# Optimization experiments

Hardware: AMD Instinct MI355X
Metric: run time of the kernel (lower is better)

## Reference

```python
import jax, jax.numpy as jnp
import numpy as np

# Modulated deformable conv2d (torchvision semantics): per kernel tap, sample the
# input at a runtime-offset location via bilinear interpolation (zero padding
# outside the image), modulate with mask, then do the weighted accumulation.

STRIDE = (1, 1)
PADDING = (1, 1)
DILATION = (1, 1)


def deform_conv2d(x, offset, mask, weight, bias):
    B, C, H, W = x.shape
    O, Cg, kh, kw = weight.shape
    K = kh * kw
    og = offset.shape[1] // (2 * K)          # offset groups
    Ho, Wo = offset.shape[2], offset.shape[3]
    sh, sw = STRIDE
    ph, pw = PADDING
    dh, dw = DILATION

    off = offset.reshape(B, og, K, 2, Ho, Wo)
    ki = jnp.arange(K)
    base_ky = ((ki // kw) * dh).astype(x.dtype)            # [K]
    base_kx = ((ki % kw) * dw).astype(x.dtype)
    base_h = (jnp.arange(Ho) * sh - ph).astype(x.dtype)    # [Ho]
    base_w = (jnp.arange(Wo) * sw - pw).astype(x.dtype)    # [Wo]
    # sampling positions, [B, og, K, Ho, Wo]
    p_y = off[:, :, :, 0] + base_ky[None, None, :, None, None] + base_h[None, None, None, :, None]
    p_x = off[:, :, :, 1] + base_kx[None, None, :, None, None] + base_w[None, None, None, None, :]

    y0 = jnp.floor(p_y)
    x0 = jnp.floor(p_x)
    ly = p_y - y0
    lx = p_x - x0
    y0i = y0.astype(jnp.int32)
    x0i = x0.astype(jnp.int32)

    Cog = C // og
    x_flat = x.reshape(B, og, Cog, H * W)

    def gather(yi, xi):
        valid = ((yi >= 0) & (yi < H) & (xi >= 0) & (xi < W))
        idx = jnp.clip(yi, 0, H - 1) * W + jnp.clip(xi, 0, W - 1)
        idx_flat = idx.reshape(B, og, 1, K * Ho * Wo)
        v = jnp.take_along_axis(x_flat, idx_flat, axis=3).reshape(B, og, Cog, K, Ho, Wo)
        return v * valid[:, :, None].astype(x.dtype)

    w00 = ((1 - ly) * (1 - lx))[:, :, None]
    w01 = ((1 - ly) * lx)[:, :, None]
    w10 = (ly * (1 - lx))[:, :, None]
    w11 = (ly * lx)[:, :, None]
    val = (w00 * gather(y0i, x0i) + w01 * gather(y0i, x0i + 1)
           + w10 * gather(y0i + 1, x0i) + w11 * gather(y0i + 1, x0i + 1))

    if mask is not None:
        val = val * mask.reshape(B, og, K, Ho, Wo)[:, :, None]

    # grouped conv accumulation over sampled taps
    G = C // Cg                               # conv groups (=1 here)
    val = val.reshape(B, G, C // G, K, Ho, Wo)
    w = weight.reshape(G, O // G, Cg, K)
    out = jnp.einsum('bgckhw,gock->bgohw', val, w).reshape(B, O, Ho, Wo)
    if bias is not None:
        out = out + bias[None, :, None, None]
    return out


def setup_inputs() -> dict:
    key = jax.random.key(0)
    k1, k2, k3, k4, k5 = jax.random.split(key, 5)
    B, C, H, W = 4, 64, 128, 128
    O, kh, kw = 64, 3, 3
    return {
        'input': jax.random.normal(k1, (B, C, H, W), dtype=jnp.float32),
        'offset': jax.random.normal(k2, (B, 2 * kh * kw, H, W), dtype=jnp.float32),
        'mask': jax.random.uniform(k3, (B, kh * kw, H, W), dtype=jnp.float32),
        'weight': jax.random.normal(k4, (O, C, kh, kw), dtype=jnp.float32) * (1.0 / np.sqrt(C * kh * kw)),
        'bias': jax.random.normal(k5, (O,), dtype=jnp.float32) * 0.01,
    }


def reference(input, offset, mask, weight, bias):
    return deform_conv2d(input, offset, mask, weight, bias)
```

## Files before the change

kernel.cpp:

```cpp
#include <hip/hip_runtime.h>


#define BB 4
#define CC 64
#define HH 128
#define WW 128
#define OO 64
#define KHW 3
#define KK 9
#define HW (HH * WW)

typedef __bf16 bf16_t;
typedef bf16_t bf16x8 __attribute__((ext_vector_type(8)));
typedef float f32x4 __attribute__((ext_vector_type(4)));

__global__ __launch_bounds__(256) void nhwc_kernel(const float* __restrict__ x,
                                                   bf16_t* __restrict__ xt) {
    __shared__ float tile[64 * 65];
    const int t  = threadIdx.x;
    const int b  = blockIdx.x >> 8;
    const int p0 = (blockIdx.x & 255) << 6;
#pragma unroll
    for (int i = 0; i < 16; ++i) {
        int c = i * 4 + (t >> 6);
        int p = t & 63;
        tile[c * 65 + p] = x[(b * CC + c) * HW + p0 + p];
    }
    __syncthreads();
#pragma unroll
    for (int i = 0; i < 16; ++i) {
        int p = i * 4 + (t >> 6);
        int c = t & 63;
        xt[(size_t)((b * HW) + p0 + p) * CC + c] = (bf16_t)tile[c * 65 + p];
    }
}

__global__ void wfrag_kernel(const float* __restrict__ w,
                             bf16_t* __restrict__ wf) {
    int i = blockIdx.x * blockDim.x + threadIdx.x;
    if (i >= OO * CC * KK) return;
    int j    = i & 7;
    int lane = (i >> 3) & 63;
    int nt   = (i >> 9) & 3;
    int q    = (i >> 11) & 1;
    int k    = i >> 12;
    int o = nt * 16 + (lane & 15);
    int c = q * 32 + ((lane >> 4) << 3) + j;
    wf[i] = (bf16_t)w[(o * CC + c) * KK + k];
}

__global__ __launch_bounds__(256, 2) void deform_conv_mfma(
    const bf16_t* __restrict__ xt, const float* __restrict__ offset,
    const float* __restrict__ mask, const bf16x8* __restrict__ wf,
    const float* __restrict__ bias, float* __restrict__ out) {
    const int t    = threadIdx.x;
    const int b    = blockIdx.x >> 8;
    const int p0   = (blockIdx.x & 255) << 6;
    const int lane = t & 63;
    const int wv   = t >> 6;
    const int m0   = wv << 4;
    const int col  = lane & 15;
    const int quad = lane >> 4;

    const int rem = p0 + m0 + col;
    const int ho  = rem >> 7;
    const int wo  = rem & (WW - 1);
    const int chq = quad << 3;

    const bf16_t* xb = xt + (size_t)b * HW * CC;

    f32x4 acc[4];
#pragma unroll
    for (int nt = 0; nt < 4; ++nt) acc[nt] = (f32x4){0.f, 0.f, 0.f, 0.f};

    for (int k = 0; k < KK; ++k) {
        float offy = offset[((b * (2 * KK) + 2 * k) * HW) + rem];
        float offx = offset[((b * (2 * KK) + 2 * k + 1) * HW) + rem];
        float mm   = mask[((b * KK + k) * HW) + rem];
        float py = offy + (float)(k / KHW) + (float)(ho - 1);
        float px = offx + (float)(k % KHW) + (float)(wo - 1);
        float fy0 = floorf(py), fx0 = floorf(px);
        float ly = py - fy0, lx = px - fx0;
        int y0 = (int)fy0, x0 = (int)fx0;
        int y1 = y0 + 1, x1 = x0 + 1;
        bool vy0 = (y0 >= 0) && (y0 < HH);
        bool vy1 = (y1 >= 0) && (y1 < HH);
        bool vx0 = (x0 >= 0) && (x0 < WW);
        bool vx1 = (x1 >= 0) && (x1 < WW);
        int cy0 = min(max(y0, 0), HH - 1), cy1 = min(max(y1, 0), HH - 1);
        int cx0 = min(max(x0, 0), WW - 1), cx1 = min(max(x1, 0), WW - 1);
        float w0 = (vy0 && vx0) ? mm * (1.0f - ly) * (1.0f - lx) : 0.0f;
        float w1 = (vy0 && vx1) ? mm * (1.0f - ly) * lx : 0.0f;
        float w2 = (vy1 && vx0) ? mm * ly * (1.0f - lx) : 0.0f;
        float w3 = (vy1 && vx1) ? mm * ly * lx : 0.0f;

        const bf16_t* c00 = xb + (cy0 * WW + cx0) * CC + chq;
        const bf16_t* c01 = xb + (cy0 * WW + cx1) * CC + chq;
        const bf16_t* c10 = xb + (cy1 * WW + cx0) * CC + chq;
        const bf16_t* c11 = xb + (cy1 * WW + cx1) * CC + chq;

        bf16x8 a00 = *(const bf16x8*)(c00);
        bf16x8 a01 = *(const bf16x8*)(c01);
        bf16x8 a02 = *(const bf16x8*)(c10);
        bf16x8 a03 = *(const bf16x8*)(c11);
        bf16x8 a10 = *(const bf16x8*)(c00 + 32);
        bf16x8 a11 = *(const bf16x8*)(c01 + 32);
        bf16x8 a12 = *(const bf16x8*)(c10 + 32);
        bf16x8 a13 = *(const bf16x8*)(c11 + 32);

        bf16x8 af0, af1;
#pragma unroll
        for (int i = 0; i < 8; ++i) {
            float v = w0 * (float)a00[i] + w1 * (float)a01[i] +
                      w2 * (float)a02[i] + w3 * (float)a03[i];
            af0[i] = (bf16_t)v;
        }
#pragma unroll
        for (int i = 0; i < 8; ++i) {
            float v = w0 * (float)a10[i] + w1 * (float)a11[i] +
                      w2 * (float)a12[i] + w3 * (float)a13[i];
            af1[i] = (bf16_t)v;
        }

        const bf16x8* wk = wf + (size_t)(k * 8) * 64;
#pragma unroll
        for (int nt = 0; nt < 4; ++nt) {
            bf16x8 b0 = wk[nt * 64 + lane];
            acc[nt] = __builtin_amdgcn_mfma_f32_16x16x32_bf16(af0, b0, acc[nt],
                                                              0, 0, 0);
        }
#pragma unroll
        for (int nt = 0; nt < 4; ++nt) {
            bf16x8 b1 = wk[(4 + nt) * 64 + lane];
            acc[nt] = __builtin_amdgcn_mfma_f32_16x16x32_bf16(af1, b1, acc[nt],
                                                              0, 0, 0);
        }
    }

#pragma unroll
    for (int nt = 0; nt < 4; ++nt) {
        int o = nt * 16 + col;
        float bv = bias[o];
        f32x4 r = acc[nt];
        r.x += bv; r.y += bv; r.z += bv; r.w += bv;
        float* dst = out + (size_t)(b * OO + o) * HW + p0 + m0 + quad * 4;
        *(f32x4*)dst = r;
    }
}

extern "C" void kernel_launch(void* const* d_in, const int* in_sizes, int n_in,
                              void* d_out, int out_size, void* d_ws,
                              size_t ws_size, hipStream_t stream) {
    const float* x      = (const float*)d_in[0];
    const float* offset = (const float*)d_in[1];
    const float* mask   = (const float*)d_in[2];
    const float* weight = (const float*)d_in[3];
    const float* bias   = (const float*)d_in[4];
    float* out = (float*)d_out;

    bf16_t* xt  = (bf16_t*)d_ws;
    bf16_t* wfr = (bf16_t*)((char*)d_ws + (size_t)BB * HW * CC * 2);

    nhwc_kernel<<<BB * (HW / 64), 256, 0, stream>>>(x, xt);

    int nw = OO * CC * KK;
    wfrag_kernel<<<(nw + 255) / 256, 256, 0, stream>>>(weight, wfr);

    deform_conv_mfma<<<BB * (HW / 64), 256, 0, stream>>>(
        xt, offset, mask, (const bf16x8*)wfr, bias, out);
}
```

Baseline: 124.0 us.

## Split channel halves across waves with LDS reduction and prefetch offsets

```diff
diff --git a/kernel.cpp b/kernel.cpp
--- a/kernel.cpp
+++ b/kernel.cpp
@@ -49,34 +49,41 @@
     wf[i] = (bf16_t)w[(o * CC + c) * KK + k];
 }
 
-__global__ __launch_bounds__(256, 2) void deform_conv_mfma(
+__global__ __launch_bounds__(256, 4) void deform_conv_mfma(
     const bf16_t* __restrict__ xt, const float* __restrict__ offset,
     const float* __restrict__ mask, const bf16x8* __restrict__ wf,
     const float* __restrict__ bias, float* __restrict__ out) {
-    const int t    = threadIdx.x;
-    const int b    = blockIdx.x >> 8;
-    const int p0   = (blockIdx.x & 255) << 6;
-    const int lane = t & 63;
-    const int wv   = t >> 6;
-    const int m0   = wv << 4;
-    const int col  = lane & 15;
-    const int quad = lane >> 4;
+    const int t     = threadIdx.x;
+    const int lane  = t & 63;
+    const int wv    = t >> 6;
+    const int strip = wv & 1;
+    const int half  = wv >> 1;
+    const int b     = blockIdx.x >> 9;
+    const int p0    = (blockIdx.x & 511) << 5;
+    const int m0    = strip << 4;
+    const int col   = lane & 15;
+    const int quad  = lane >> 4;
 
     const int rem = p0 + m0 + col;
     const int ho  = rem >> 7;
     const int wo  = rem & (WW - 1);
-    const int chq = quad << 3;
+    const int cb  = (half << 5) + (quad << 3);
 
     const bf16_t* xb = xt + (size_t)b * HW * CC;
+
+    __shared__ f32x4 red[2][4][64];
 
     f32x4 acc[4];
 #pragma unroll
     for (int nt = 0; nt < 4; ++nt) acc[nt] = (f32x4){0.f, 0.f, 0.f, 0.f};
 
+    const int offbase = (b * (2 * KK)) * HW + rem;
+    const int mbase   = (b * KK) * HW + rem;
+    float offy = offset[offbase];
+    float offx = offset[offbase + HW];
+    float mm   = mask[mbase];
+
     for (int k = 0; k < KK; ++k) {
-        float offy = offset[((b * (2 * KK) + 2 * k) * HW) + rem];
-        float offx = offset[((b * (2 * KK) + 2 * k + 1) * HW) + rem];
-        float mm   = mask[((b * KK + k) * HW) + rem];
         float py = offy + (float)(k / KHW) + (float)(ho - 1);
         float px = offx + (float)(k % KHW) + (float)(wo - 1);
         float fy0 = floorf(py), fx0 = floorf(px);
@@ -94,57 +101,52 @@
         float w2 = (vy1 && vx0) ? mm * ly * (1.0f - lx) : 0.0f;
         float w3 = (vy1 && vx1) ? mm * ly * lx : 0.0f;
 
-        const bf16_t* c00 = xb + (cy0 * WW + cx0) * CC + chq;
-        const bf16_t* c01 = xb + (cy0 * WW + cx1) * CC + chq;
-        const bf16_t* c10 = xb + (cy1 * WW + cx0) * CC + chq;
-        const bf16_t* c11 = xb + (cy1 * WW + cx1) * CC + chq;
+        bf16x8 a0 = *(const bf16x8*)(xb + (cy0 * WW + cx0) * CC + cb);
+        bf16x8 a1 = *(const bf16x8*)(xb + (cy0 * WW + cx1) * CC + cb);
+        bf16x8 a2 = *(const bf16x8*)(xb + (cy1 * WW + cx0) * CC + cb);
+        bf16x8 a3 = *(const bf16x8*)(xb + (cy1 * WW + cx1) * CC + cb);
 
-        bf16x8 a00 = *(const bf16x8*)(c00);
-        bf16x8 a01 = *(const bf16x8*)(c01);
-        bf16x8 a02 = *(const bf16x8*)(c10);
-        bf16x8 a03 = *(const bf16x8*)(c11);
-        bf16x8 a10 = *(const bf16x8*)(c00 + 32);
-        bf16x8 a11 = *(const bf16x8*)(c01 + 32);
-        bf16x8 a12 = *(const bf16x8*)(c10 + 32);
-        bf16x8 a13 = *(const bf16x8*)(c11 + 32);
+        float offy_n = 0.f, offx_n = 0.f, mm_n = 0.f;
+        if (k + 1 < KK) {
+            offy_n = offset[offbase + (2 * k + 2) * HW];
+            offx_n = offset[offbase + (2 * k + 3) * HW];
+            mm_n   = mask[mbase + (k + 1) * HW];
+        }
 
-        bf16x8 af0, af1;
+        bf16x8 af;
 #pragma unroll
         for (int i = 0; i < 8; ++i) {
-            float v = w0 * (float)a00[i] + w1 * (float)a01[i] +
-                      w2 * (float)a02[i] + w3 * (float)a03[i];
-            af0[i] = (bf16_t)v;
-        }
-#pragma unroll
-        for (int i = 0; i < 8; ++i) {
-            float v = w0 * (float)a10[i] + w1 * (float)a11[i] +
-                      w2 * (float)a12[i] + w3 * (float)a13[i];
-            af1[i] = (bf16_t)v;
+            float v = w0 * (float)a0[i] + w1 * (float)a1[i] +
+                      w2 * (float)a2[i] + w3 * (float)a3[i];
+            af[i] = (bf16_t)v;
         }
 
-        const bf16x8* wk = wf + (size_t)(k * 8) * 64;
+        const bf16x8* wk = wf + (size_t)((k * 2 + half) * 4) * 64;
 #pragma unroll
         for (int nt = 0; nt < 4; ++nt) {
-            bf16x8 b0 = wk[nt * 64 + lane];
-            acc[nt] = __builtin_amdgcn_mfma_f32_16x16x32_bf16(af0, b0, acc[nt],
+            bf16x8 bfr = wk[nt * 64 + lane];
+            acc[nt] = __builtin_amdgcn_mfma_f32_16x16x32_bf16(af, bfr, acc[nt],
                                                               0, 0, 0);
         }
+
+        offy = offy_n; offx = offx_n; mm = mm_n;
+    }
+
+    if (half == 1) {
+#pragma unroll
+        for (int nt = 0; nt < 4; ++nt) red[strip][nt][lane] = acc[nt];
+    }
+    __syncthreads();
+    if (half == 0) {
 #pragma unroll
         for (int nt = 0; nt < 4; ++nt) {
-            bf16x8 b1 = wk[(4 + nt) * 64 + lane];
-            acc[nt] = __builtin_amdgcn_mfma_f32_16x16x32_bf16(af1, b1, acc[nt],
-                                                              0, 0, 0);
+            int o = nt * 16 + col;
+            float bv = bias[o];
+            f32x4 r = acc[nt] + red[strip][nt][lane];
+            r.x += bv; r.y += bv; r.z += bv; r.w += bv;
+            float* dst = out + (size_t)(b * OO + o) * HW + p0 + m0 + quad * 4;
+            *(f32x4*)dst = r;
         }
-    }
-
-#pragma unroll
-    for (int nt = 0; nt < 4; ++nt) {
-        int o = nt * 16 + col;
-        float bv = bias[o];
-        f32x4 r = acc[nt];
-        r.x += bv; r.y += bv; r.z += bv; r.w += bv;
-        float* dst = out + (size_t)(b * OO + o) * HW + p0 + m0 + quad * 4;
-        *(f32x4*)dst = r;
     }
 }
 
@@ -166,6 +168,6 @@
     int nw = OO * CC * KK;
     wfrag_kernel<<<(nw + 255) / 256, 256, 0, stream>>>(weight, wfr);
 
-    deform_conv_mfma<<<BB * (HW / 64), 256, 0, stream>>>(
+    deform_conv_mfma<<<BB * (HW / 32), 256, 0, stream>>>(
         xt, offset, mask, (const bf16x8*)wfr, bias, out);
 }
```

Measured after the change: 123.4 us. No clear change (-0.5%).
